# Performance work log

Hardware: AMD Instinct MI355X
Metric: run time of the kernel (lower is better)

The kernel has to match this reference:

```python
import jax, jax.numpy as jnp
import numpy as np

N = 50000
E = 1600000
IN_DIM = 128
HID = 32
HEADS = 4
OUT = 32
NEG_SLOPE = 0.2


def gat_conv(h, src, dst, W, al, ar, b, n_heads, d_out):
    # h: [N, F_in]; W: [F_in, H*D]; al/ar: [H, D]; b: [H*D]
    n = h.shape[0]
    z = (h @ W).reshape(n, n_heads, d_out)            # [N,H,D]
    el = (z * al[None]).sum(-1)                        # [N,H]
    er = (z * ar[None]).sum(-1)                        # [N,H]
    e = el[src] + er[dst]                              # [E,H]
    e = jnp.where(e > 0, e, NEG_SLOPE * e)             # leaky_relu(0.2)
    # edge softmax grouped by destination node
    m = jax.ops.segment_max(e, dst, num_segments=n)    # [N,H]
    ex = jnp.exp(e - m[dst])                           # [E,H]
    s = jax.ops.segment_sum(ex, dst, num_segments=n)   # [N,H]
    alpha = ex / s[dst]                                # [E,H]
    msg = alpha[:, :, None] * z[src]                   # [E,H,D]
    out = jax.ops.segment_sum(msg, dst, num_segments=n)  # [N,H,D]
    return out + b.reshape(1, n_heads, d_out)


def setup_inputs() -> dict:
    key = jax.random.key(0)
    ks = jax.random.split(key, 12)
    h = jax.random.normal(ks[0], (N, IN_DIM), dtype=jnp.float32)
    src = jax.random.randint(ks[1], (E,), 0, N, dtype=jnp.int32)
    dst = jax.random.randint(ks[2], (E,), 0, N, dtype=jnp.int32)
    s1 = 1.0 / np.sqrt(IN_DIM)
    W1 = jax.random.uniform(ks[3], (IN_DIM, HEADS * HID), jnp.float32, -s1, s1)
    al1 = jax.random.normal(ks[4], (HEADS, HID), jnp.float32) * 0.1
    ar1 = jax.random.normal(ks[5], (HEADS, HID), jnp.float32) * 0.1
    b1 = jnp.zeros((HEADS * HID,), jnp.float32)
    f2 = HEADS * HID
    s2 = 1.0 / np.sqrt(f2)
    W2 = jax.random.uniform(ks[6], (f2, OUT), jnp.float32, -s2, s2)
    al2 = jax.random.normal(ks[7], (1, OUT), jnp.float32) * 0.1
    ar2 = jax.random.normal(ks[8], (1, OUT), jnp.float32) * 0.1
    b2 = jnp.zeros((OUT,), jnp.float32)
    return {"h": h, "src": src, "dst": dst, "W1": W1, "al1": al1, "ar1": ar1,
            "b1": b1, "W2": W2, "al2": al2, "ar2": ar2, "b2": b2}


def reference(h, src, dst, W1, al1, ar1, b1, W2, al2, ar2, b2):
    x = gat_conv(h, src, dst, W1, al1, ar1, b1, HEADS, HID)  # [N,H,D]
    x = x.reshape(N, HEADS * HID)                             # flatten(1)
    x = jax.nn.elu(x)                                         # act
    y = gat_conv(x, src, dst, W2, al2, ar2, b2, 1, OUT)       # [N,1,OUT]
    return y.squeeze(1)                                        # [N,OUT]
```

## Files before the change

### kernel.cpp

```cpp
#include <hip/hip_runtime.h>
#include <hip/hip_fp16.h>

#define NN 50000
#define NEG_SLOPE 0.2f
#define BSHIFT 9
#define BNODES (1 << BSHIFT)
#define NBUCK ((NN + BNODES - 1) >> BSHIFT)
#define BCAP 18432

typedef _Float16 f16x4 __attribute__((ext_vector_type(4)));
typedef _Float16 f16x8 __attribute__((ext_vector_type(8)));
typedef float    f32x4 __attribute__((ext_vector_type(4)));
typedef unsigned int u32x4 __attribute__((ext_vector_type(4)));

__global__ void zero_kernel(unsigned* bucket_cursor, int* src_sorted_pad) {
    int i = threadIdx.x;
    if (i < NBUCK) bucket_cursor[i] = (unsigned)(i * BCAP);
    if (i < 64) src_sorted_pad[i] = 0;
}

__global__ __launch_bounds__(1024) void bucketA(
        const int* __restrict__ src, const int* __restrict__ dst,
        unsigned* __restrict__ bucket_cursor, int2* __restrict__ ebuf, int E) {
    __shared__ unsigned hist[NBUCK];
    int tid = threadIdx.x;
    if (tid < NBUCK) hist[tid] = 0u;
    __syncthreads();
    int e = blockIdx.x * 1024 + tid;
    int s = 0, d = 0, b = 0;
    bool valid = e < E;
    if (valid) {
        s = src[e]; d = dst[e]; b = d >> BSHIFT;
        atomicAdd(&hist[b], 1u);
    }
    __syncthreads();
    if (tid < NBUCK) {
        unsigned c = hist[tid];
        hist[tid] = c ? atomicAdd(&bucket_cursor[tid], c) : 0u;
    }
    __syncthreads();
    if (valid) {
        unsigned slot = atomicAdd(&hist[b], 1u);
        ebuf[slot] = make_int2(s, d);
    }
}

__global__ __launch_bounds__(512) void gemm1_mfma(
        const float* __restrict__ h, const float* __restrict__ W1,
        const float* __restrict__ al1, const float* __restrict__ ar1,
        __half* __restrict__ z1h, float* __restrict__ el1, float* __restrict__ er1, int N) {
    __shared__ alignas(16) __half hA[128 * 128];
    __shared__ alignas(16) __half Bt[128 * 128];
    int tid = threadIdx.x;
    int lane = tid & 63, w = tid >> 6;
    int row0 = blockIdx.x * 128;
    int nrow = min(128, N - row0);

    for (int idx = tid; idx < 128 * 32; idx += 512) {
        int row = idx >> 5, kq = idx & 31;
        float4 v = (row < nrow) ? ((const float4*)(h + (size_t)(row0 + row) * 128))[kq]
                                : make_float4(0.f, 0.f, 0.f, 0.f);
        f16x4 hv;
        hv[0] = (_Float16)v.x; hv[1] = (_Float16)v.y;
        hv[2] = (_Float16)v.z; hv[3] = (_Float16)v.w;
        int off = row * 256 + ((kq * 8) ^ ((row & 15) << 4));
        *(f16x4*)((char*)hA + off) = hv;
    }
    {
        int col = tid & 127, kg = tid >> 7;
        #pragma unroll
        for (int it = 0; it < 4; ++it) {
            int k0 = it * 32 + kg * 8;
            f16x8 wv;
            #pragma unroll
            for (int i = 0; i < 8; ++i)
                wv[i] = (_Float16)W1[(size_t)(k0 + i) * 128 + col];
            int off = col * 256 + ((k0 * 2) ^ ((col & 15) << 4));
            *(f16x8*)((char*)Bt + off) = wv;
        }
    }
    __syncthreads();

    f32x4 acc[8];
    #pragma unroll
    for (int ct = 0; ct < 8; ++ct) acc[ct] = (f32x4){0.f, 0.f, 0.f, 0.f};

    int arow = w * 16 + (lane & 15);
    int kbyte_lane = ((lane >> 4) * 8) * 2;
    #pragma unroll
    for (int ks = 0; ks < 4; ++ks) {
        int kb = ks * 64 + kbyte_lane;
        f16x8 a = *(const f16x8*)((const char*)hA + arow * 256 + (kb ^ ((arow & 15) << 4)));
        #pragma unroll
        for (int ct = 0; ct < 8; ++ct) {
            int col = ct * 16 + (lane & 15);
            f16x8 b = *(const f16x8*)((const char*)Bt + col * 256 + (kb ^ ((col & 15) << 4)));
            acc[ct] = __builtin_amdgcn_mfma_f32_16x16x32_f16(a, b, acc[ct], 0, 0, 0);
        }
    }

    int lrow = (lane >> 4) * 4;
    #pragma unroll
    for (int ct = 0; ct < 8; ++ct) {
        int col = ct * 16 + (lane & 15);
        #pragma unroll
        for (int r = 0; r < 4; ++r) {
            int rl = w * 16 + lrow + r;
            if (rl < nrow)
                z1h[(size_t)(row0 + rl) * 128 + col] = __float2half(acc[ct][r]);
        }
    }
    #pragma unroll
    for (int hh = 0; hh < 4; ++hh) {
        int c0 = hh * 32 + (lane & 15);
        float a_l0 = al1[c0], a_l1 = al1[c0 + 16];
        float a_r0 = ar1[c0], a_r1 = ar1[c0 + 16];
        #pragma unroll
        for (int r = 0; r < 4; ++r) {
            float v0 = acc[2 * hh][r], v1 = acc[2 * hh + 1][r];
            float pl = v0 * a_l0 + v1 * a_l1;
            float pr = v0 * a_r0 + v1 * a_r1;
            #pragma unroll
            for (int o = 8; o; o >>= 1) {
                pl += __shfl_xor(pl, o, 16);
                pr += __shfl_xor(pr, o, 16);
            }
            int rl = w * 16 + lrow + r;
            if ((lane & 15) == 0 && rl < nrow) {
                el1[(row0 + rl) * 4 + hh] = pl;
                er1[(row0 + rl) * 4 + hh] = pr;
            }
        }
    }
}

__global__ __launch_bounds__(1024) void scatterC(
        const int2* __restrict__ ebuf, const unsigned* __restrict__ bucket_cursor,
        const float* __restrict__ el1, const float* __restrict__ er1,
        unsigned* __restrict__ off, int* __restrict__ src_sorted,
        uint2* __restrict__ alpha1p, int N, int E) {
    __shared__ unsigned hist[BNODES], nodeoff[BNODES], wsum[8], bsz[128];
    __shared__ float4 er_s[BNODES];
    int b = blockIdx.x, tid = threadIdx.x;
    int base = b << BSHIFT;
    unsigned rs = (unsigned)(b * BCAP), re = bucket_cursor[b];
    const float4* el1v = (const float4*)el1;
    const float4* er1v = (const float4*)er1;

    if (tid < 128) bsz[tid] = (tid < NBUCK) ? bucket_cursor[tid] - (unsigned)(tid * BCAP) : 0u;
    if (tid < BNODES) {
        hist[tid] = 0u;
        int n = base + tid;
        er_s[tid] = (n < N) ? er1v[n] : make_float4(0.f, 0.f, 0.f, 0.f);
    }
    __syncthreads();
    if (tid == 0) {
        unsigned r = 0;
        for (int t = 0; t < NBUCK; ++t) { unsigned c = bsz[t]; bsz[t] = r; r += c; }
        if (b == 0) off[N] = (unsigned)E;
    }
    __syncthreads();
    unsigned boff = bsz[b];

    for (unsigned i = rs + tid; i < re; i += 1024)
        atomicAdd(&hist[ebuf[i].y - base], 1u);
    __syncthreads();
    unsigned v = 0, x = 0;
    int lane = tid & 63, wv = tid >> 6;
    if (tid < BNODES) {
        v = hist[tid]; x = v;
        #pragma unroll
        for (int o = 1; o < 64; o <<= 1) {
            unsigned n = __shfl_up(x, o, 64);
            if (lane >= o) x += n;
        }
        if (lane == 63) wsum[wv] = x;
    }
    __syncthreads();
    if (tid == 0) {
        unsigned r = 0;
        #pragma unroll
        for (int k = 0; k < 8; ++k) { unsigned t = wsum[k]; wsum[k] = r; r += t; }
    }
    __syncthreads();
    if (tid < BNODES) {
        unsigned exoff = x - v + wsum[wv] + boff;
        nodeoff[tid] = exoff;
        if (base + tid < N) off[base + tid] = exoff;
        hist[tid] = 0u;
    }
    __syncthreads();
    for (unsigned i = rs + tid; i < re; i += 1024) {
        int2 ed = ebuf[i];
        int ln = ed.y - base;
        unsigned r = atomicAdd(&hist[ln], 1u);
        unsigned p = nodeoff[ln] + r;
        src_sorted[p] = ed.x;
        float4 el = el1v[ed.x];
        float4 er = er_s[ln];
        float v0 = el.x + er.x; v0 = fmaxf(v0, NEG_SLOPE * v0);
        float v1 = el.y + er.y; v1 = fmaxf(v1, NEG_SLOPE * v1);
        float v2 = el.z + er.z; v2 = fmaxf(v2, NEG_SLOPE * v2);
        float v3 = el.w + er.w; v3 = fmaxf(v3, NEG_SLOPE * v3);
        union { __half2 h2[2]; uint2 u; } pk;
        pk.h2[0] = __floats2half2_rn(__expf(v0), __expf(v1));
        pk.h2[1] = __floats2half2_rn(__expf(v2), __expf(v3));
        alpha1p[p] = pk.u;
    }
}

__global__ __launch_bounds__(256) void agg1_spmm(
        const int* __restrict__ src_sorted, const unsigned* __restrict__ off,
        const __half* __restrict__ alpha1h, const __half* __restrict__ z1h,
        const float* __restrict__ b1, __half* __restrict__ x) {
    int tid = threadIdx.x, lane = tid & 63, w = tid >> 6;
    int node = blockIdx.x * 4 + w;
    int start = (int)off[node], end = (int)off[node + 1];
    int g = lane >> 4, l16 = lane & 15, head = l16 >> 2;
    const char* zbase = (const char*)z1h + (unsigned)(l16 * 16);
    const unsigned short* au = (const unsigned short*)alpha1h;

    float acc[8];
    #pragma unroll
    for (int jj = 0; jj < 8; ++jj) acc[jj] = 0.f;
    float sloc = 0.f;
    for (int base = start; base < end; base += 32) {
        #pragma unroll
        for (int t = 0; t < 8; ++t) {
            int i = base + 4 * t + g;
            int s = __builtin_nontemporal_load(src_sorted + i);
            unsigned short us = __builtin_nontemporal_load(au + ((unsigned)i * 4u + head));
            __half ah = *reinterpret_cast<__half*>(&us);
            float a = __half2float(ah);
            a = (i < end) ? a : 0.f;
            sloc += a;
            float4 r = *(const float4*)(zbase + ((unsigned)s << 8));
            const __half* zh = (const __half*)&r;
            #pragma unroll
            for (int k = 0; k < 8; ++k)
                acc[k] = fmaf(__half2float(zh[k]), a, acc[k]);
        }
    }
    #pragma unroll
    for (int jj = 0; jj < 8; ++jj) {
        acc[jj] += __shfl_xor(acc[jj], 16, 64);
        acc[jj] += __shfl_xor(acc[jj], 32, 64);
    }
    sloc += __shfl_xor(sloc, 16, 64);
    sloc += __shfl_xor(sloc, 32, 64);
    float inv = sloc > 0.f ? 1.f / sloc : 0.f;

    if (g == 0) {
        float xv[8];
        #pragma unroll
        for (int jj = 0; jj < 8; ++jj) {
            float t = acc[jj] * inv + b1[l16 * 8 + jj];
            xv[jj] = t > 0.f ? t : (__expf(t) - 1.f);
        }
        union { __half2 h2[4]; u32x4 u; } pk;
        #pragma unroll
        for (int k = 0; k < 4; ++k) pk.h2[k] = __floats2half2_rn(xv[2 * k], xv[2 * k + 1]);
        __builtin_nontemporal_store(pk.u, (u32x4*)(x + ((size_t)node << 7) + l16 * 8));
    }
}

__global__ __launch_bounds__(256) void gemm2el_kernel(
        const __half* __restrict__ x, const float* __restrict__ W2,
        const float* __restrict__ al2, const float* __restrict__ ar2,
        __half* __restrict__ z2h, float* __restrict__ el2, float* __restrict__ er2, int N) {
    __shared__ __half xsh[64][136];
    __shared__ float W2T[32][132];
    int tid = threadIdx.x;
    int row0 = blockIdx.x * 64;
    int nrow = min(64, N - row0);

    for (int idx = tid; idx < nrow * 16; idx += 256) {
        int r = idx >> 4, kq = idx & 15;
        float4 v = ((const float4*)(x + (size_t)(row0 + r) * 128))[kq];
        *(float4*)&xsh[r][kq * 8] = v;
    }
    for (int idx = tid; idx < 4096; idx += 256) {
        int k = idx >> 5, c = idx & 31;
        W2T[c][k] = W2[idx];
    }
    __syncthreads();

    int gc = tid & 15, gr = tid >> 4;
    float acc[4][2];
    #pragma unroll
    for (int j = 0; j < 4; ++j) { acc[j][0] = 0.f; acc[j][1] = 0.f; }

    for (int p = 0; p < 32; ++p) {
        float4 w0 = *(const float4*)&W2T[gc][p * 4];
        float4 w1 = *(const float4*)&W2T[gc + 16][p * 4];
        #pragma unroll
        for (int j = 0; j < 4; ++j) {
            const __half* xr = &xsh[gr * 4 + j][p * 4];
            float x0 = __half2float(xr[0]), x1 = __half2float(xr[1]);
            float x2 = __half2float(xr[2]), x3 = __half2float(xr[3]);
            acc[j][0] = fmaf(x0, w0.x, fmaf(x1, w0.y, fmaf(x2, w0.z, fmaf(x3, w0.w, acc[j][0]))));
            acc[j][1] = fmaf(x0, w1.x, fmaf(x1, w1.y, fmaf(x2, w1.z, fmaf(x3, w1.w, acc[j][1]))));
        }
    }

    float al0 = al2[gc], al1v = al2[gc + 16];
    float ar0 = ar2[gc], ar1v = ar2[gc + 16];
    #pragma unroll
    for (int j = 0; j < 4; ++j) {
        int r = gr * 4 + j;
        int node = row0 + r;
        bool live = r < nrow;
        if (live) {
            z2h[(size_t)node * 32 + gc]      = __float2half(acc[j][0]);
            z2h[(size_t)node * 32 + gc + 16] = __float2half(acc[j][1]);
        }
        float pl = acc[j][0] * al0 + acc[j][1] * al1v;
        float pr = acc[j][0] * ar0 + acc[j][1] * ar1v;
        #pragma unroll
        for (int o = 8; o; o >>= 1) {
            pl += __shfl_xor(pl, o, 16);
            pr += __shfl_xor(pr, o, 16);
        }
        if (live && gc == 0) { el2[node] = pl; er2[node] = pr; }
    }
}

__global__ __launch_bounds__(256) void agg2_fused(
        const int* __restrict__ src_sorted, const unsigned* __restrict__ off,
        const float* __restrict__ el2, const float* __restrict__ er2,
        const __half* __restrict__ z2h, const float* __restrict__ b2,
        float* __restrict__ out) {
    int tid = threadIdx.x, lane = tid & 63;
    int node = blockIdx.x * 4 + (tid >> 6);
    int start = (int)off[node], end = (int)off[node + 1];
    float er_d = er2[node];

    int g = lane >> 2, l4 = lane & 3;
    const char* zbase = (const char*)z2h + (unsigned)(l4 * 16);
    float acc[8];
    #pragma unroll
    for (int jj = 0; jj < 8; ++jj) acc[jj] = 0.f;
    float sloc = 0.f;
    for (int base = start; base < end; base += 64) {
        #pragma unroll
        for (int t = 0; t < 4; ++t) {
            int i = base + 16 * t + g;
            int s = __builtin_nontemporal_load(src_sorted + i);
            float v = el2[s] + er_d;
            v = fmaxf(v, NEG_SLOPE * v);
            float ex = __expf(v);
            ex = (i < end) ? ex : 0.f;
            sloc += ex;
            float4 r = *(const float4*)(zbase + ((unsigned)s << 6));
            const __half* zh = (const __half*)&r;
            #pragma unroll
            for (int k = 0; k < 8; ++k)
                acc[k] = fmaf(__half2float(zh[k]), ex, acc[k]);
        }
    }
    #pragma unroll
    for (int jj = 0; jj < 8; ++jj) {
        acc[jj] += __shfl_xor(acc[jj], 4, 64);
        acc[jj] += __shfl_xor(acc[jj], 8, 64);
        acc[jj] += __shfl_xor(acc[jj], 16, 64);
        acc[jj] += __shfl_xor(acc[jj], 32, 64);
    }
    sloc += __shfl_xor(sloc, 4, 64);
    sloc += __shfl_xor(sloc, 8, 64);
    sloc += __shfl_xor(sloc, 16, 64);
    sloc += __shfl_xor(sloc, 32, 64);
    float inv = sloc > 0.f ? 1.f / sloc : 0.f;
    if (g == 0) {
        #pragma unroll
        for (int jj = 0; jj < 8; ++jj)
            out[(size_t)node * 32 + l4 * 8 + jj] = acc[jj] * inv + b2[l4 * 8 + jj];
    }
}

extern "C" void kernel_launch(void* const* d_in, const int* in_sizes, int n_in,
                              void* d_out, int out_size, void* d_ws, size_t ws_size,
                              hipStream_t stream) {
    const float* h   = (const float*)d_in[0];
    const int*   src = (const int*)d_in[1];
    const int*   dst = (const int*)d_in[2];
    const float* W1  = (const float*)d_in[3];
    const float* al1 = (const float*)d_in[4];
    const float* ar1 = (const float*)d_in[5];
    const float* b1  = (const float*)d_in[6];
    const float* W2  = (const float*)d_in[7];
    const float* al2 = (const float*)d_in[8];
    const float* ar2 = (const float*)d_in[9];
    const float* b2  = (const float*)d_in[10];
    float* out = (float*)d_out;
    const int N = NN;
    const int E = in_sizes[1];

    char* w = (char*)d_ws;
    __half* z1h       = (__half*)w;   w += (size_t)N * 128 * 2;
    __half* z2h       = (__half*)w;   w += (size_t)N * 32 * 2;
    __half* xh        = (__half*)w;   w += (size_t)N * 128 * 2;
    int2*  ebuf       = (int2*)w;     w += (size_t)NBUCK * BCAP * 8;
    uint2* alpha1p    = (uint2*)w;    w += ((size_t)E + 32) * 8;
    int*   src_sorted = (int*)w;      w += ((size_t)E + 64) * 4;
    float* el1        = (float*)w;    w += (size_t)N * 4 * 4;
    float* er1        = (float*)w;    w += (size_t)N * 4 * 4;
    float* el2        = (float*)w;    w += (size_t)N * 4;
    float* er2        = (float*)w;    w += (size_t)N * 4;
    unsigned* off     = (unsigned*)w; w += (size_t)(N + 16) * 4;
    unsigned* bucket_cursor = (unsigned*)w; w += 128 * 4;

    zero_kernel<<<1, 128, 0, stream>>>(bucket_cursor, src_sorted + E);
    bucketA<<<(E + 1023) / 1024, 1024, 0, stream>>>(src, dst, bucket_cursor, ebuf, E);
    gemm1_mfma<<<(N + 127) / 128, 512, 0, stream>>>(h, W1, al1, ar1, z1h, el1, er1, N);
    scatterC<<<NBUCK, 1024, 0, stream>>>(ebuf, bucket_cursor, el1, er1,
                                         off, src_sorted, alpha1p, N, E);
    agg1_spmm<<<N / 4, 256, 0, stream>>>(src_sorted, off, (const __half*)alpha1p, z1h, b1, xh);
    gemm2el_kernel<<<(N + 63) / 64, 256, 0, stream>>>(xh, W2, al2, ar2, z2h, el2, er2, N);
    agg2_fused<<<N / 4, 256, 0, stream>>>(src_sorted, off, el2, er2, z2h, b2, out);
}
```

Baseline: 300.3 us.

## Recompute layer-1 attention logits in aggregation instead of materializing per-edge alpha

The scatter kernel no longer gathers el1 per edge, computes leaky-relu/exp, or writes a packed fp16 alpha array. The layer-1 aggregation kernel now gathers el1[src] per edge, adds the destination's er1, and computes the exponent inline, matching the layer-2 kernel. This removes an E-sized fp16x4 write and re-read plus a random gather inside the sort stage, at the cost of an extra random 4-byte gather and an exp in the aggregation loop. Nontemporal load/store hints on src_sorted and the x output are also replaced by plain accesses.

```diff
diff --git a/kernel.cpp b/kernel.cpp
--- a/kernel.cpp
+++ b/kernel.cpp
@@ -11,7 +11,6 @@
 typedef _Float16 f16x4 __attribute__((ext_vector_type(4)));
 typedef _Float16 f16x8 __attribute__((ext_vector_type(8)));
 typedef float    f32x4 __attribute__((ext_vector_type(4)));
-typedef unsigned int u32x4 __attribute__((ext_vector_type(4)));
 
 __global__ void zero_kernel(unsigned* bucket_cursor, int* src_sorted_pad) {
     int i = threadIdx.x;
@@ -136,23 +135,14 @@
 
 __global__ __launch_bounds__(1024) void scatterC(
         const int2* __restrict__ ebuf, const unsigned* __restrict__ bucket_cursor,
-        const float* __restrict__ el1, const float* __restrict__ er1,
-        unsigned* __restrict__ off, int* __restrict__ src_sorted,
-        uint2* __restrict__ alpha1p, int N, int E) {
+        unsigned* __restrict__ off, int* __restrict__ src_sorted, int N, int E) {
     __shared__ unsigned hist[BNODES], nodeoff[BNODES], wsum[8], bsz[128];
-    __shared__ float4 er_s[BNODES];
     int b = blockIdx.x, tid = threadIdx.x;
     int base = b << BSHIFT;
     unsigned rs = (unsigned)(b * BCAP), re = bucket_cursor[b];
-    const float4* el1v = (const float4*)el1;
-    const float4* er1v = (const float4*)er1;
 
     if (tid < 128) bsz[tid] = (tid < NBUCK) ? bucket_cursor[tid] - (unsigned)(tid * BCAP) : 0u;
-    if (tid < BNODES) {
-        hist[tid] = 0u;
-        int n = base + tid;
-        er_s[tid] = (n < N) ? er1v[n] : make_float4(0.f, 0.f, 0.f, 0.f);
-    }
+    if (tid < BNODES) hist[tid] = 0u;
     __syncthreads();
     if (tid == 0) {
         unsigned r = 0;
@@ -194,31 +184,20 @@
         int2 ed = ebuf[i];
         int ln = ed.y - base;
         unsigned r = atomicAdd(&hist[ln], 1u);
-        unsigned p = nodeoff[ln] + r;
-        src_sorted[p] = ed.x;
-        float4 el = el1v[ed.x];
-        float4 er = er_s[ln];
-        float v0 = el.x + er.x; v0 = fmaxf(v0, NEG_SLOPE * v0);
-        float v1 = el.y + er.y; v1 = fmaxf(v1, NEG_SLOPE * v1);
-        float v2 = el.z + er.z; v2 = fmaxf(v2, NEG_SLOPE * v2);
-        float v3 = el.w + er.w; v3 = fmaxf(v3, NEG_SLOPE * v3);
-        union { __half2 h2[2]; uint2 u; } pk;
-        pk.h2[0] = __floats2half2_rn(__expf(v0), __expf(v1));
-        pk.h2[1] = __floats2half2_rn(__expf(v2), __expf(v3));
-        alpha1p[p] = pk.u;
+        src_sorted[nodeoff[ln] + r] = ed.x;
     }
 }
 
 __global__ __launch_bounds__(256) void agg1_spmm(
         const int* __restrict__ src_sorted, const unsigned* __restrict__ off,
-        const __half* __restrict__ alpha1h, const __half* __restrict__ z1h,
-        const float* __restrict__ b1, __half* __restrict__ x) {
+        const float* __restrict__ el1, const float* __restrict__ er1,
+        const __half* __restrict__ z1h, const float* __restrict__ b1, __half* __restrict__ x) {
     int tid = threadIdx.x, lane = tid & 63, w = tid >> 6;
     int node = blockIdx.x * 4 + w;
     int start = (int)off[node], end = (int)off[node + 1];
     int g = lane >> 4, l16 = lane & 15, head = l16 >> 2;
     const char* zbase = (const char*)z1h + (unsigned)(l16 * 16);
-    const unsigned short* au = (const unsigned short*)alpha1h;
+    float er_d = er1[node * 4 + head];
 
     float acc[8];
     #pragma unroll
@@ -228,17 +207,18 @@
         #pragma unroll
         for (int t = 0; t < 8; ++t) {
             int i = base + 4 * t + g;
-            int s = __builtin_nontemporal_load(src_sorted + i);
-            unsigned short us = __builtin_nontemporal_load(au + ((unsigned)i * 4u + head));
-            __half ah = *reinterpret_cast<__half*>(&us);
-            float a = __half2float(ah);
-            a = (i < end) ? a : 0.f;
-            sloc += a;
+            int s = src_sorted[i];
+            float el = el1[(unsigned)s * 4u + head];
+            float v = el + er_d;
+            v = fmaxf(v, NEG_SLOPE * v);
+            float ex = __expf(v);
+            ex = (i < end) ? ex : 0.f;
+            sloc += ex;
             float4 r = *(const float4*)(zbase + ((unsigned)s << 8));
             const __half* zh = (const __half*)&r;
             #pragma unroll
             for (int k = 0; k < 8; ++k)
-                acc[k] = fmaf(__half2float(zh[k]), a, acc[k]);
+                acc[k] = fmaf(__half2float(zh[k]), ex, acc[k]);
         }
     }
     #pragma unroll
@@ -257,10 +237,10 @@
             float t = acc[jj] * inv + b1[l16 * 8 + jj];
             xv[jj] = t > 0.f ? t : (__expf(t) - 1.f);
         }
-        union { __half2 h2[4]; u32x4 u; } pk;
+        union { __half2 h2[4]; uint4 u; } pk;
         #pragma unroll
         for (int k = 0; k < 4; ++k) pk.h2[k] = __floats2half2_rn(xv[2 * k], xv[2 * k + 1]);
-        __builtin_nontemporal_store(pk.u, (u32x4*)(x + ((size_t)node << 7) + l16 * 8));
+        *(uint4*)(x + ((size_t)node << 7) + l16 * 8) = pk.u;
     }
 }
 
@@ -345,7 +325,7 @@
         #pragma unroll
         for (int t = 0; t < 4; ++t) {
             int i = base + 16 * t + g;
-            int s = __builtin_nontemporal_load(src_sorted + i);
+            int s = src_sorted[i];
             float v = el2[s] + er_d;
             v = fmaxf(v, NEG_SLOPE * v);
             float ex = __expf(v);
@@ -400,7 +380,6 @@
     __half* z2h       = (__half*)w;   w += (size_t)N * 32 * 2;
     __half* xh        = (__half*)w;   w += (size_t)N * 128 * 2;
     int2*  ebuf       = (int2*)w;     w += (size_t)NBUCK * BCAP * 8;
-    uint2* alpha1p    = (uint2*)w;    w += ((size_t)E + 32) * 8;
     int*   src_sorted = (int*)w;      w += ((size_t)E + 64) * 4;
     float* el1        = (float*)w;    w += (size_t)N * 4 * 4;
     float* er1        = (float*)w;    w += (size_t)N * 4 * 4;
@@ -412,9 +391,8 @@
     zero_kernel<<<1, 128, 0, stream>>>(bucket_cursor, src_sorted + E);
     bucketA<<<(E + 1023) / 1024, 1024, 0, stream>>>(src, dst, bucket_cursor, ebuf, E);
     gemm1_mfma<<<(N + 127) / 128, 512, 0, stream>>>(h, W1, al1, ar1, z1h, el1, er1, N);
-    scatterC<<<NBUCK, 1024, 0, stream>>>(ebuf, bucket_cursor, el1, er1,
-                                         off, src_sorted, alpha1p, N, E);
-    agg1_spmm<<<N / 4, 256, 0, stream>>>(src_sorted, off, (const __half*)alpha1p, z1h, b1, xh);
+    scatterC<<<NBUCK, 1024, 0, stream>>>(ebuf, bucket_cursor, off, src_sorted, N, E);
+    agg1_spmm<<<N / 4, 256, 0, stream>>>(src_sorted, off, el1, er1, z1h, b1, xh);
     gemm2el_kernel<<<(N + 63) / 64, 256, 0, stream>>>(xh, W2, al2, ar2, z2h, el2, er2, N);
     agg2_fused<<<N / 4, 256, 0, stream>>>(src_sorted, off, el2, er2, z2h, b2, out);
 }
```

Result: faster. 267.6 us (-10.9%).
